# Optimization experiments

Hardware: AMD Instinct MI355X
Metric: run time of the kernel (lower is better)

The kernel has to match this reference:

```python
import jax, jax.numpy as jnp
from jax import lax
import numpy as np

TEMPERATURE = 100.0
UNROLL = 1000
N = 2048


def setup_inputs() -> dict:
    key = jax.random.key(0)
    # kaiming_uniform_(a=sqrt(5)) on an NxN matrix -> U(-b, b) with b = sqrt(6/((1+5)*N)) = 1/sqrt(N)
    bound = 1.0 / np.sqrt(N)
    matrix = jax.random.uniform(key, (N, N), dtype=jnp.float32, minval=-bound, maxval=bound)
    return {"matrix": matrix}


def reference(matrix):
    n = matrix.shape[0]
    # numerically-shifted exponential: exp(T * (M - rowmax))
    m = jnp.exp(TEMPERATURE * (matrix - jnp.max(matrix, axis=1, keepdims=True)))

    def sinkhorn_step(m, _):
        m = m / jnp.sum(m, axis=1, keepdims=True)  # row normalize
        m = m / jnp.sum(m, axis=0, keepdims=True)  # col normalize
        return m, None

    m, _ = lax.scan(sinkhorn_step, m, None, length=UNROLL)

    lower = jnp.tril(jnp.ones((n, n), dtype=matrix.dtype))
    # output_lower = (M @ L @ M^T)^T
    output_lower = (m @ lower @ m.T).T
    return output_lower
```

## Files before the change

kernel.cpp:

```cpp
#include <hip/hip_runtime.h>

#define NN 2048
#define ITERS 1000
#define NBLK 256
#define RPW 8
#define EPS 3e-3f

typedef __attribute__((ext_vector_type(4))) float floatx4;
typedef unsigned long long u64;

#define AGENT __HIP_MEMORY_SCOPE_AGENT

static __device__ __forceinline__ void agstore64(u64* p, u64 v) {
  __hip_atomic_store(p, v, __ATOMIC_RELAXED, AGENT);
}
static __device__ __forceinline__ u64 agload64(const u64* p) {
  return __hip_atomic_load(p, __ATOMIC_RELAXED, AGENT);
}
static __device__ __forceinline__ u64 pack(float f, unsigned tag) {
  return ((u64)tag << 32) | (u64)__float_as_uint(f);
}

static __device__ __forceinline__ void poll8(const u64* rec, int tid,
                                             unsigned tag, float* x) {
  const u64* base = rec + tid * 8;
  unsigned got = 0;
  while (got != 0xFFu) {
#pragma unroll
    for (int j = 0; j < 8; j++)
      if (!(got & (1u << j))) {
        u64 wv = agload64(base + j);
        if ((unsigned)(wv >> 32) == tag) {
          x[j] = __uint_as_float((unsigned)wv);
          got |= 1u << j;
        }
      }
  }
}

static __device__ __forceinline__ void gather64(const u64* rec, int tid,
                                                float* vec, unsigned tag) {
  float x[8];
  poll8(rec, tid, tag, x);
#pragma unroll
  for (int j = 0; j < 8; j++) vec[tid * 8 + j] = x[j];
  __syncthreads();
}

static __device__ __forceinline__ bool gather64_check(const u64* rec, int tid,
                                                      float* vec, unsigned tag,
                                                      float* pv) {
  float x[8];
  poll8(rec, tid, tag, x);
  float resid = 0.f;
#pragma unroll
  for (int j = 0; j < 8; j++) {
    resid = fmaxf(resid, fabsf(x[j] / pv[j] - 1.0f));
    pv[j] = x[j];
    vec[tid * 8 + j] = x[j];
  }
  return __syncthreads_and(resid < EPS) != 0;
}

__global__ __launch_bounds__(256) void sinkhorn_kernel(
    const float* __restrict__ M, u64* recR, u64* recU, u64* recV,
    unsigned char* __restrict__ Pb, unsigned char* __restrict__ Wb)
{
  __shared__ float rowsA[RPW][NN];
  __shared__ float colsA[RPW][NN];
  __shared__ float vec[NN];
  __shared__ float myu[RPW];

  const int g = blockIdx.x;
  const int tid = threadIdx.x;
  const int w = tid >> 6;
  const int lane = tid & 63;
  const int r0 = 2 * w, r1 = r0 + 1;

  {
    const float4* src = (const float4*)(M + (size_t)g * RPW * NN);
    float4* dst = (float4*)&rowsA[0][0];
    for (int c = tid; c < RPW * NN / 4; c += 256) dst[c] = src[c];
  }
  __syncthreads();

  float m0 = -3.4e38f, m1 = -3.4e38f;
  for (int k = lane; k < NN; k += 64) {
    m0 = fmaxf(m0, rowsA[r0][k]);
    m1 = fmaxf(m1, rowsA[r1][k]);
  }
  for (int off = 32; off; off >>= 1) {
    m0 = fmaxf(m0, __shfl_xor(m0, off, 64));
    m1 = fmaxf(m1, __shfl_xor(m1, off, 64));
  }
  if (lane == 0) {
    agstore64(&recR[RPW * g + r0], pack(m0, 1));
    agstore64(&recR[RPW * g + r1], pack(m1, 1));
  }

  float4 sx0[8], sx1[8];
#pragma unroll
  for (int rr = 0; rr < 8; rr++) {
    const float* src = M + (size_t)(tid * 8 + rr) * NN + RPW * g;
    sx0[rr] = *(const float4*)src;
    sx1[rr] = *(const float4*)(src + 4);
  }

  float s0 = 0.f, s1 = 0.f;
  for (int k = lane; k < NN; k += 64) {
    float e0 = __expf(100.0f * (rowsA[r0][k] - m0));
    float e1 = __expf(100.0f * (rowsA[r1][k] - m1));
    rowsA[r0][k] = e0;
    rowsA[r1][k] = e1;
    s0 += e0;
    s1 += e1;
  }
  for (int off = 32; off; off >>= 1) {
    s0 += __shfl_xor(s0, off, 64);
    s1 += __shfl_xor(s1, off, 64);
  }
  {
    float u0 = 1.0f / s0, u1 = 1.0f / s1;
    if (lane == 0) {
      agstore64(&recU[RPW * g + r0], pack(u0, 2));
      agstore64(&recU[RPW * g + r1], pack(u1, 2));
      myu[r0] = u0;
      myu[r1] = u1;
    }
  }

  {
    float rm[8];
    poll8(recR, tid, 1, rm);
#pragma unroll
    for (int rr = 0; rr < 8; rr++) {
      int i = tid * 8 + rr;
      colsA[0][i] = __expf(100.0f * (sx0[rr].x - rm[rr]));
      colsA[1][i] = __expf(100.0f * (sx0[rr].y - rm[rr]));
      colsA[2][i] = __expf(100.0f * (sx0[rr].z - rm[rr]));
      colsA[3][i] = __expf(100.0f * (sx0[rr].w - rm[rr]));
      colsA[4][i] = __expf(100.0f * (sx1[rr].x - rm[rr]));
      colsA[5][i] = __expf(100.0f * (sx1[rr].y - rm[rr]));
      colsA[6][i] = __expf(100.0f * (sx1[rr].z - rm[rr]));
      colsA[7][i] = __expf(100.0f * (sx1[rr].w - rm[rr]));
    }
  }

  float pv[8];
#pragma unroll
  for (int j = 0; j < 8; j++) pv[j] = 1.0f;

  gather64(recU, tid, vec, 2);
  {
    float t0 = 0.f, t1 = 0.f;
#pragma unroll 8
    for (int k = lane; k < NN; k += 64) {
      float uu = vec[k];
      t0 += colsA[r0][k] * uu;
      t1 += colsA[r1][k] * uu;
    }
    for (int off = 32; off; off >>= 1) {
      t0 += __shfl_xor(t0, off, 64);
      t1 += __shfl_xor(t1, off, 64);
    }
    if (lane == 0) {
      agstore64(&recV[RPW * g + r0], pack(1.0f / t0, 3));
      agstore64(&recV[RPW * g + r1], pack(1.0f / t1, 3));
    }
  }

  bool done = false;
  unsigned utag = 4;
  for (int it = 1; it < ITERS; it++, utag += 2) {
    if (gather64_check(recV, tid, vec, utag - 1, pv)) { done = true; break; }
    float a0 = 0.f, a1 = 0.f;
#pragma unroll 8
    for (int k = lane; k < NN; k += 64) {
      float vv = vec[k];
      a0 += rowsA[r0][k] * vv;
      a1 += rowsA[r1][k] * vv;
    }
    for (int off = 32; off; off >>= 1) {
      a0 += __shfl_xor(a0, off, 64);
      a1 += __shfl_xor(a1, off, 64);
    }
    {
      float u0 = 1.0f / a0, u1 = 1.0f / a1;
      if (lane == 0) {
        agstore64(&recU[RPW * g + r0], pack(u0, utag));
        agstore64(&recU[RPW * g + r1], pack(u1, utag));
        myu[r0] = u0;
        myu[r1] = u1;
      }
    }

    gather64(recU, tid, vec, utag);
    float t0 = 0.f, t1 = 0.f;
#pragma unroll 8
    for (int k = lane; k < NN; k += 64) {
      float uu = vec[k];
      t0 += colsA[r0][k] * uu;
      t1 += colsA[r1][k] * uu;
    }
    for (int off = 32; off; off >>= 1) {
      t0 += __shfl_xor(t0, off, 64);
      t1 += __shfl_xor(t1, off, 64);
    }
    if (lane == 0) {
      agstore64(&recV[RPW * g + r0], pack(1.0f / t0, utag + 1));
      agstore64(&recV[RPW * g + r1], pack(1.0f / t1, utag + 1));
    }
  }
  if (!done) gather64(recV, tid, vec, 2 * ITERS + 1);

  for (int idx = tid; idx < RPW * NN / 2; idx += 256) {
    int r = idx >> 10, j2 = (idx & 1023) * 2;
    float p0 = 256.0f * myu[r] * rowsA[r][j2] * vec[j2];
    float p1 = 256.0f * myu[r] * rowsA[r][j2 + 1] * vec[j2 + 1];
    int pk = __builtin_amdgcn_cvt_pk_fp8_f32(p0, p1, 0, false);
    ((unsigned short*)Pb)[((((size_t)(RPW * g + r)) << 11) | j2) >> 1] = (unsigned short)pk;
  }
  for (int rr = 0; rr < 2; rr++) {
    int r = 2 * w + rr;
    float ur = myu[r];
    int base = lane * 32;
    float cs = 0.f;
    for (int t = 0; t < 32; t++) {
      int k = base + ((t + lane) & 31);
      cs += ur * rowsA[r][k] * vec[k];
    }
    float s = cs;
    for (int off = 1; off < 64; off <<= 1) {
      float t = __shfl_down(s, off, 64);
      if (lane + off < 64) s += t;
    }
    float run = __shfl_down(s, 1, 64);
    if (lane == 63) run = 0.f;
    float wv[32];
#pragma unroll
    for (int k = 31; k >= 0; k--) {
      int kk = base + k;
      run += ur * rowsA[r][kk] * vec[kk];
      wv[k] = run;
    }
#pragma unroll
    for (int pq = 0; pq < 16; pq++) {
      int pk = __builtin_amdgcn_cvt_pk_fp8_f32(wv[2 * pq], wv[2 * pq + 1], 0, false);
      ((unsigned short*)Wb)[((((size_t)(RPW * g + r)) << 11) | (base + 2 * pq)) >> 1] =
          (unsigned short)pk;
    }
  }
}

#define BM 128
#define BN 64

__global__ __launch_bounds__(256) void gemm_nt_fp8(const unsigned char* __restrict__ P,
                                                   const unsigned char* __restrict__ W,
                                                   float* __restrict__ out)
{
  __shared__ unsigned char As[BM * 64];
  __shared__ unsigned char Bs[BN * 64];
  const int tid = threadIdx.x;
  const int w = tid >> 6, lane = tid & 63;
  const int quad = lane >> 4, l16 = lane & 15;
  const int i0 = blockIdx.y * BM, j0 = blockIdx.x * BN;
  const int wr = (w >> 1) * 64;
  const int wc = (w & 1) * 32;

  const int lrow = lane >> 2;
  const int lp2 = (lane & 3) * 2;

  floatx4 acc[4][2] = {};

  for (int k0 = 0; k0 < NN; k0 += 64) {
#pragma unroll
    for (int c = 0; c < 3; c++) {
      int q = w * 3 + c;
      const unsigned char* gsrc;
      unsigned char* ldst;
      if (q < 8) {
        int row = q * 16 + lrow;
        gsrc = P + (size_t)(i0 + row) * NN + k0 + ((lp2 ^ (row & 6)) * 8);
        ldst = As + q * 1024;
      } else {
        int q2 = q - 8;
        int row = q2 * 16 + lrow;
        gsrc = W + (size_t)(j0 + row) * NN + k0 + ((lp2 ^ (row & 6)) * 8);
        ldst = Bs + q2 * 1024;
      }
      __builtin_amdgcn_global_load_lds(
          (const __attribute__((address_space(1))) void*)gsrc,
          (__attribute__((address_space(3))) void*)ldst, 16, 0, 0);
    }
    __syncthreads();

#pragma unroll
    for (int kc = 0; kc < 2; kc++) {
      long a[4], b[2];
      int cg = kc * 4 + quad;
#pragma unroll
      for (int mt = 0; mt < 4; mt++) {
        int r = wr + mt * 16 + l16;
        a[mt] = *(const long*)(As + r * 64 + ((cg ^ (r & 6)) * 8));
      }
#pragma unroll
      for (int nt = 0; nt < 2; nt++) {
        int r = wc + nt * 16 + l16;
        b[nt] = *(const long*)(Bs + r * 64 + ((cg ^ (r & 6)) * 8));
      }
#pragma unroll
      for (int mt = 0; mt < 4; mt++)
#pragma unroll
        for (int nt = 0; nt < 2; nt++)
          acc[mt][nt] = __builtin_amdgcn_mfma_f32_16x16x32_fp8_fp8(a[mt], b[nt], acc[mt][nt], 0, 0, 0);
    }
    __syncthreads();
  }

#pragma unroll
  for (int mt = 0; mt < 4; mt++)
#pragma unroll
    for (int nt = 0; nt < 2; nt++)
#pragma unroll
      for (int e = 0; e < 4; e++) {
        int row = i0 + wr + mt * 16 + quad * 4 + e;
        int col = j0 + wc + nt * 16 + l16;
        out[(size_t)row * NN + col] = acc[mt][nt][e] * 0.00390625f;
      }
}

extern "C" void kernel_launch(void* const* d_in, const int* in_sizes, int n_in,
                              void* d_out, int out_size, void* d_ws, size_t ws_size,
                              hipStream_t stream) {
  const float* M = (const float*)d_in[0];
  float* out = (float*)d_out;
  char* ws = (char*)d_ws;

  u64* recR = (u64*)(ws + 4096);
  u64* recU = (u64*)(ws + 4096 + 16384);
  u64* recV = (u64*)(ws + 4096 + 32768);
  unsigned char* Pb = (unsigned char*)(ws + (1u << 20));
  unsigned char* Wb = (unsigned char*)(ws + (1u << 20) + (8u << 20));

  hipMemsetAsync(ws + 4096, 0, 49152, stream);

  sinkhorn_kernel<<<dim3(NBLK), dim3(256), 0, stream>>>(M, recR, recU, recV, Pb, Wb);
  gemm_nt_fp8<<<dim3(NN / BN, NN / BM), dim3(256), 0, stream>>>(Pb, Wb, out);
}
```

Measured before the change: 137.3 us.

## Give each wave its own 64x32 GEMM tile with double-buffered async LDS loads

The FP8 GEMM drops block-shared tiles and __syncthreads. Each wavefront now owns an independent 64x32 output tile, keeps private double-buffered LDS staging, and uses vmcnt waits to prefetch the K-slice two steps ahead. This is meant to remove block-wide barriers and overlap global loads with MFMA work. In exchange, operands are no longer shared across waves, which raises global/L2 traffic and LDS footprint (48KB per block).

```diff
diff --git a/kernel.cpp b/kernel.cpp
--- a/kernel.cpp
+++ b/kernel.cpp
@@ -252,70 +252,80 @@
   }
 }
 
-#define BM 128
-#define BN 64
-
 __global__ __launch_bounds__(256) void gemm_nt_fp8(const unsigned char* __restrict__ P,
                                                    const unsigned char* __restrict__ W,
                                                    float* __restrict__ out)
 {
-  __shared__ unsigned char As[BM * 64];
-  __shared__ unsigned char Bs[BN * 64];
+  __shared__ unsigned char SA[4][2][4096];
+  __shared__ unsigned char SB[4][2][2048];
   const int tid = threadIdx.x;
   const int w = tid >> 6, lane = tid & 63;
   const int quad = lane >> 4, l16 = lane & 15;
-  const int i0 = blockIdx.y * BM, j0 = blockIdx.x * BN;
-  const int wr = (w >> 1) * 64;
-  const int wc = (w & 1) * 32;
+
+  const int t = blockIdx.x * 4 + w;
+  const int i0 = (t & 31) * 64;
+  const int j0 = (t >> 5) * 32;
 
   const int lrow = lane >> 2;
   const int lp2 = (lane & 3) * 2;
 
   floatx4 acc[4][2] = {};
 
-  for (int k0 = 0; k0 < NN; k0 += 64) {
-#pragma unroll
-    for (int c = 0; c < 3; c++) {
-      int q = w * 3 + c;
-      const unsigned char* gsrc;
-      unsigned char* ldst;
-      if (q < 8) {
-        int row = q * 16 + lrow;
-        gsrc = P + (size_t)(i0 + row) * NN + k0 + ((lp2 ^ (row & 6)) * 8);
-        ldst = As + q * 1024;
-      } else {
-        int q2 = q - 8;
-        int row = q2 * 16 + lrow;
-        gsrc = W + (size_t)(j0 + row) * NN + k0 + ((lp2 ^ (row & 6)) * 8);
-        ldst = Bs + q2 * 1024;
-      }
+  auto issue = [&](int k0, int b) {
+#pragma unroll
+    for (int c = 0; c < 4; c++) {
+      int row = c * 16 + lrow;
+      const unsigned char* gsrc =
+          P + (size_t)(i0 + row) * NN + k0 + ((lp2 ^ (row & 6)) * 8);
       __builtin_amdgcn_global_load_lds(
           (const __attribute__((address_space(1))) void*)gsrc,
-          (__attribute__((address_space(3))) void*)ldst, 16, 0, 0);
-    }
-    __syncthreads();
+          (__attribute__((address_space(3))) void*)(&SA[w][b][c * 1024]), 16, 0, 0);
+    }
+#pragma unroll
+    for (int c = 0; c < 2; c++) {
+      int row = c * 16 + lrow;
+      const unsigned char* gsrc =
+          W + (size_t)(j0 + row) * NN + k0 + ((lp2 ^ (row & 6)) * 8);
+      __builtin_amdgcn_global_load_lds(
+          (const __attribute__((address_space(1))) void*)gsrc,
+          (__attribute__((address_space(3))) void*)(&SB[w][b][c * 1024]), 16, 0, 0);
+    }
+  };
+
+  issue(0, 0);
+  issue(64, 1);
+
+  for (int k0 = 0; k0 < NN; k0 += 64) {
+    const int b = (k0 >> 6) & 1;
+    __builtin_amdgcn_s_waitcnt(0x0F76);
+    asm volatile("" ::: "memory");
 
 #pragma unroll
     for (int kc = 0; kc < 2; kc++) {
-      long a[4], b[2];
+      long a[4], b2[2];
       int cg = kc * 4 + quad;
 #pragma unroll
       for (int mt = 0; mt < 4; mt++) {
-        int r = wr + mt * 16 + l16;
-        a[mt] = *(const long*)(As + r * 64 + ((cg ^ (r & 6)) * 8));
+        int r = mt * 16 + l16;
+        a[mt] = *(const long*)(&SA[w][b][r * 64 + ((cg ^ (r & 6)) * 8)]);
       }
 #pragma unroll
       for (int nt = 0; nt < 2; nt++) {
-        int r = wc + nt * 16 + l16;
-        b[nt] = *(const long*)(Bs + r * 64 + ((cg ^ (r & 6)) * 8));
+        int r = nt * 16 + l16;
+        b2[nt] = *(const long*)(&SB[w][b][r * 64 + ((cg ^ (r & 6)) * 8)]);
       }
 #pragma unroll
       for (int mt = 0; mt < 4; mt++)
 #pragma unroll
         for (int nt = 0; nt < 2; nt++)
-          acc[mt][nt] = __builtin_amdgcn_mfma_f32_16x16x32_fp8_fp8(a[mt], b[nt], acc[mt][nt], 0, 0, 0);
-    }
-    __syncthreads();
+          acc[mt][nt] = __builtin_amdgcn_mfma_f32_16x16x32_fp8_fp8(a[mt], b2[nt], acc[mt][nt], 0, 0, 0);
+    }
+
+    if (k0 + 128 < NN) {
+      __builtin_amdgcn_s_waitcnt(0xC07F);
+      asm volatile("" ::: "memory");
+      issue(k0 + 128, b);
+    }
   }
 
 #pragma unroll
@@ -324,8 +334,8 @@
     for (int nt = 0; nt < 2; nt++)
 #pragma unroll
       for (int e = 0; e < 4; e++) {
-        int row = i0 + wr + mt * 16 + quad * 4 + e;
-        int col = j0 + wc + nt * 16 + l16;
+        int row = i0 + mt * 16 + quad * 4 + e;
+        int col = j0 + nt * 16 + l16;
         out[(size_t)row * NN + col] = acc[mt][nt][e] * 0.00390625f;
       }
 }
@@ -346,5 +356,5 @@
   hipMemsetAsync(ws + 4096, 0, 49152, stream);
 
   sinkhorn_kernel<<<dim3(NBLK), dim3(256), 0, stream>>>(M, recR, recU, recV, Pb, Wb);
-  gemm_nt_fp8<<<dim3(NN / BN, NN / BM), dim3(256), 0, stream>>>(Pb, Wb, out);
-}
+  gemm_nt_fp8<<<dim3(512), dim3(256), 0, stream>>>(Pb, Wb, out);
+}
```

After: 136.5 us. About the same (-0.6%).
